# Kernel tuning notes

Hardware: AMD Instinct MI355X
Metric: run time of the kernel (lower is better)

## Reference

```python
import jax, jax.numpy as jnp
import numpy as np

HIDDEN = 2048
HEADS = 16
HEAD_DIM = HIDDEN // HEADS          # 128
HALF = HEAD_DIM // 2                # 64
LATENT = HIDDEN // 4                # 512 (compression_ratio=4)
ROPE_BASE = 10000.0


def _rope_cos_sin(seq_len):
    # LlamaRotaryEmbedding with dim=HALF
    inv_freq = 1.0 / (ROPE_BASE ** (jnp.arange(0, HALF, 2, dtype=jnp.float32) / HALF))
    t = jnp.arange(seq_len, dtype=jnp.float32)
    freqs = jnp.einsum('i,j->ij', t, inv_freq)          # [S, HALF/2]
    emb = jnp.concatenate([freqs, freqs], axis=-1)       # [S, HALF]
    cos = jnp.cos(emb)[None, :, None, :]                 # [1,S,1,HALF]
    sin = jnp.sin(emb)[None, :, None, :]
    return cos, sin


def _rotate_half(x):
    x1, x2 = jnp.split(x, 2, axis=-1)
    return jnp.concatenate([-x2, x1], axis=-1)


def _apply_rope(x, cos, sin):
    return x * cos + _rotate_half(x) * sin


def setup_inputs() -> dict:
    key = jax.random.key(0)
    ks = jax.random.split(key, 10)
    B, S = 2, 2048
    std = 0.02
    inp = {
        'x':        jax.random.normal(ks[0], (B, S, HIDDEN), jnp.float32),
        # weights stored as [in, out] (transposed torch Linear weight)
        'W_kv_d':   jax.random.normal(ks[1], (HIDDEN, LATENT), jnp.float32) * std,
        'W_q_d':    jax.random.normal(ks[2], (HIDDEN, LATENT), jnp.float32) * std,
        'W_k_u':    jax.random.normal(ks[3], (LATENT, HEADS * HALF), jnp.float32) * std,
        'W_q_u':    jax.random.normal(ks[4], (LATENT, HEADS * HALF), jnp.float32) * std,
        'W_v_u':    jax.random.normal(ks[5], (LATENT, HIDDEN), jnp.float32) * std,
        'W_rope_k': jax.random.normal(ks[6], (HIDDEN, HIDDEN // 2), jnp.float32) * std,
        'W_rope_q': jax.random.normal(ks[7], (LATENT, HIDDEN // 2), jnp.float32) * std,
        'W_o':      jax.random.normal(ks[8], (HIDDEN, HIDDEN), jnp.float32) * std,
    }
    return inp


def reference(x, W_kv_d, W_q_d, W_k_u, W_q_u, W_v_u, W_rope_k, W_rope_q, W_o):
    B, S, _ = x.shape
    kv_latent = x @ W_kv_d                      # [B,S,LATENT]
    q_latent = x @ W_q_d                        # [B,S,LATENT]

    k = (kv_latent @ W_k_u).reshape(B, S, HEADS, HALF)
    q = (q_latent @ W_q_u).reshape(B, S, HEADS, HALF)
    v = (kv_latent @ W_v_u).reshape(B, S, HEADS, HEAD_DIM)

    q_rope = (q_latent @ W_rope_q).reshape(B, S, HEADS, HALF)
    k_rope = (x @ W_rope_k).reshape(B, S, HEADS, HALF)

    cos, sin = _rope_cos_sin(S)
    k_rope = _apply_rope(k_rope, cos, sin)
    q_rope = _apply_rope(q_rope, cos, sin)

    q = jnp.concatenate([q, q_rope], axis=-1)   # [B,S,H,HEAD_DIM]
    k = jnp.concatenate([k, k_rope], axis=-1)

    scale = 1.0 / jnp.sqrt(jnp.float32(HEAD_DIM))
    scores = jnp.einsum('bqhd,bkhd->bhqk', q, k) * scale   # [B,H,S,S]
    causal = jnp.tril(jnp.ones((S, S), dtype=bool))
    scores = jnp.where(causal[None, None], scores, jnp.float32(-1e30))
    attn = jax.nn.softmax(scores, axis=-1)
    y = jnp.einsum('bhqk,bkhd->bqhd', attn, v).reshape(B, S, HIDDEN)
    return y @ W_o
```

## Files before the change

kernel.cpp:

```cpp
#include <hip/hip_runtime.h>
#include <hip/hip_bf16.h>

typedef __hip_bfloat16 bf16;
typedef __attribute__((ext_vector_type(8))) short short8;
typedef __attribute__((ext_vector_type(4))) float f32x4;

#define AS1 __attribute__((address_space(1)))
#define AS3 __attribute__((address_space(3)))

__device__ __forceinline__ void gload_lds16(const bf16* gp, bf16* lp) {
  __builtin_amdgcn_global_load_lds((const AS1 void*)gp, (AS3 void*)lp, 16, 0, 0);
}

__device__ __forceinline__ float fast_exp2(float x) {
#if __has_builtin(__builtin_amdgcn_exp2f)
  return __builtin_amdgcn_exp2f(x);
#else
  return exp2f(x);
#endif
}

__device__ __forceinline__ void store_c(bf16* C, size_t idx, float v) { C[idx] = __float2bfloat16(v); }
__device__ __forceinline__ void store_c(float* C, size_t idx, float v) { C[idx] = v; }

struct __align__(8) b16x4 { bf16 a, b, c, d; };

__global__ void cvt_f32_bf16(const float* __restrict__ in, bf16* __restrict__ out) {
  const int i = (blockIdx.x * 256 + threadIdx.x) * 4;
  const float4 v = *(const float4*)(in + i);
  out[i + 0] = __float2bfloat16(v.x);
  out[i + 1] = __float2bfloat16(v.y);
  out[i + 2] = __float2bfloat16(v.z);
  out[i + 3] = __float2bfloat16(v.w);
}

struct PrepArgs {
  const float* src[8];
  bf16* dst[8];
  int R[8], C[8], cum[8];
};

__global__ void prep_kernel(PrepArgs a) {
  __shared__ bf16 t[32][33];
  const int blk = blockIdx.x;
  int e = 0;
  while (e < 7 && blk >= a.cum[e]) ++e;
  const int lt = blk - (e ? a.cum[e - 1] : 0);
  const int R = a.R[e], C = a.C[e];
  const int tpr = C >> 5;
  const int bx = lt % tpr, by = lt / tpr;
  const float* in = a.src[e];
  bf16* out = a.dst[e];
  const int c0 = bx * 32, r0 = by * 32;
  const int tx = threadIdx.x, ty = threadIdx.y;
  for (int i = 0; i < 4; ++i)
    t[ty + 8 * i][tx] = __float2bfloat16(in[(size_t)(r0 + ty + 8 * i) * C + c0 + tx]);
  __syncthreads();
  for (int i = 0; i < 4; ++i)
    out[(size_t)(c0 + ty + 8 * i) * R + r0 + tx] = t[tx][ty + 8 * i];
}

template <typename CT, int MODE>
__global__ void gemm_bt(const bf16* __restrict__ A, int lda,
                        const bf16* __restrict__ Bt,
                        CT* __restrict__ C, bf16* __restrict__ C2, int ldc,
                        int K)
{
  __shared__ __align__(16) bf16 As[128 * 32];
  __shared__ __align__(16) bf16 Bs[128 * 32];
  const int tid  = threadIdx.x;
  const int wave = tid >> 6, lane = tid & 63;
  const int quad = lane >> 4, l16 = lane & 15;
  const int m0 = blockIdx.y * 128, n0 = blockIdx.x * 128;
  const int wm = (wave >> 1) * 64, wn = (wave & 1) * 64;

  f32x4 acc[4][4];
#pragma unroll
  for (int i = 0; i < 4; ++i)
#pragma unroll
    for (int j = 0; j < 4; ++j) acc[i][j] = (f32x4){0.f, 0.f, 0.f, 0.f};

  const int r1  = tid >> 2;
  const int ks1 = (tid & 3) * 8;

  for (int k0 = 0; k0 < K; k0 += 32) {
    gload_lds16(A  + (size_t)(m0 + r1)      * lda + k0 + ks1, &As[tid * 8]);
    gload_lds16(A  + (size_t)(m0 + r1 + 64) * lda + k0 + ks1, &As[(tid + 256) * 8]);
    gload_lds16(Bt + (size_t)(n0 + r1)      * K   + k0 + ks1, &Bs[tid * 8]);
    gload_lds16(Bt + (size_t)(n0 + r1 + 64) * K   + k0 + ks1, &Bs[(tid + 256) * 8]);
    __syncthreads();

    short8 af[4], bf_[4];
#pragma unroll
    for (int mt = 0; mt < 4; ++mt)
      af[mt] = *(const short8*)&As[(wm + mt * 16 + l16) * 32 + quad * 8];
#pragma unroll
    for (int nt = 0; nt < 4; ++nt)
      bf_[nt] = *(const short8*)&Bs[(wn + nt * 16 + l16) * 32 + quad * 8];
#pragma unroll
    for (int mt = 0; mt < 4; ++mt)
#pragma unroll
      for (int nt = 0; nt < 4; ++nt)
        acc[mt][nt] = __builtin_amdgcn_mfma_f32_16x16x32_bf16(af[mt], bf_[nt], acc[mt][nt], 0, 0, 0);
    __syncthreads();
  }

#pragma unroll
  for (int mt = 0; mt < 4; ++mt) {
    const int row = m0 + wm + mt * 16 + quad * 4;
#pragma unroll
    for (int nt = 0; nt < 4; ++nt) {
      const int cn = n0 + wn + nt * 16 + l16;
      const f32x4 v = acc[mt][nt];
      if (MODE == 0) {
#pragma unroll
        for (int r = 0; r < 4; ++r)
          store_c(C, (size_t)(row + r) * ldc + cn, v[r]);
      } else if (MODE == 4) {
        if (cn < 1024) {
#pragma unroll
          for (int r = 0; r < 4; ++r)
            store_c(C, (size_t)(row + r) * 1024 + cn, v[r]);
        } else {
          const int cn2 = cn - 1024;
          const int g = ((cn2 >> 6) << 7) + 64 + (cn2 & 63);
#pragma unroll
          for (int r = 0; r < 4; ++r)
            C2[(size_t)(row + r) * 2048 + g] = __float2bfloat16(v[r]);
        }
      }
    }
  }
}

__global__ void gemm_up_fused(const bf16* __restrict__ latcat,
                              const bf16* __restrict__ wtUP,
                              const bf16* __restrict__ wtQcat,
                              bf16* __restrict__ vT, bf16* __restrict__ kfull,
                              bf16* __restrict__ qfull)
{
  const bool is2 = (blockIdx.x >= 24);
  const bf16* A  = latcat + (is2 ? 512 : 0);
  const bf16* Bt = is2 ? wtQcat : wtUP;
  const int n0 = (is2 ? (int)blockIdx.x - 24 : (int)blockIdx.x) * 128;
  const int K = 512, lda = 1024;

  __shared__ __align__(16) bf16 As[128 * 32];
  __shared__ __align__(16) bf16 Bs[128 * 32];
  const int tid  = threadIdx.x;
  const int wave = tid >> 6, lane = tid & 63;
  const int quad = lane >> 4, l16 = lane & 15;
  const int m0 = blockIdx.y * 128;
  const int wm = (wave >> 1) * 64, wn = (wave & 1) * 64;

  f32x4 acc[4][4];
#pragma unroll
  for (int i = 0; i < 4; ++i)
#pragma unroll
    for (int j = 0; j < 4; ++j) acc[i][j] = (f32x4){0.f, 0.f, 0.f, 0.f};

  const int r1  = tid >> 2;
  const int ks1 = (tid & 3) * 8;

  for (int k0 = 0; k0 < K; k0 += 32) {
    gload_lds16(A  + (size_t)(m0 + r1)      * lda + k0 + ks1, &As[tid * 8]);
    gload_lds16(A  + (size_t)(m0 + r1 + 64) * lda + k0 + ks1, &As[(tid + 256) * 8]);
    gload_lds16(Bt + (size_t)(n0 + r1)      * K   + k0 + ks1, &Bs[tid * 8]);
    gload_lds16(Bt + (size_t)(n0 + r1 + 64) * K   + k0 + ks1, &Bs[(tid + 256) * 8]);
    __syncthreads();

    short8 af[4], bf_[4];
#pragma unroll
    for (int mt = 0; mt < 4; ++mt)
      af[mt] = *(const short8*)&As[(wm + mt * 16 + l16) * 32 + quad * 8];
#pragma unroll
    for (int nt = 0; nt < 4; ++nt)
      bf_[nt] = *(const short8*)&Bs[(wn + nt * 16 + l16) * 32 + quad * 8];
#pragma unroll
    for (int mt = 0; mt < 4; ++mt)
#pragma unroll
      for (int nt = 0; nt < 4; ++nt)
        acc[mt][nt] = __builtin_amdgcn_mfma_f32_16x16x32_bf16(af[mt], bf_[nt], acc[mt][nt], 0, 0, 0);
    __syncthreads();
  }

  if (is2) {
#pragma unroll
    for (int mt = 0; mt < 4; ++mt) {
      const int row = m0 + wm + mt * 16 + quad * 4;
#pragma unroll
      for (int nt = 0; nt < 4; ++nt) {
        const int cn = n0 + wn + nt * 16 + l16;
        const int g = (((cn >> 6) & 15) << 7) + ((cn >> 10) << 6) + (cn & 63);
        const f32x4 v = acc[mt][nt];
#pragma unroll
        for (int r = 0; r < 4; ++r)
          qfull[(size_t)(row + r) * 2048 + g] = __float2bfloat16(v[r]);
      }
    }
  } else {
#pragma unroll
    for (int mt = 0; mt < 4; ++mt) {
      const int row = m0 + wm + mt * 16 + quad * 4;
#pragma unroll
      for (int nt = 0; nt < 4; ++nt) {
        const int cn = n0 + wn + nt * 16 + l16;
        const f32x4 v = acc[mt][nt];
        if (cn < 1024) {
          const int g = ((cn >> 6) << 7) + (cn & 63);
#pragma unroll
          for (int r = 0; r < 4; ++r)
            kfull[(size_t)(row + r) * 2048 + g] = __float2bfloat16(v[r]);
        } else {
          const int cn2 = cn - 1024;
          const int bb = row >> 11, s0 = row & 2047;
          b16x4 pk;
          pk.a = __float2bfloat16(v[0]); pk.b = __float2bfloat16(v[1]);
          pk.c = __float2bfloat16(v[2]); pk.d = __float2bfloat16(v[3]);
          *(b16x4*)(vT + ((size_t)(bb * 2048 + cn2)) * 2048 + s0) = pk;
        }
      }
    }
  }
}

__global__ void rope_kernel(bf16* __restrict__ q, bf16* __restrict__ k)
{
  const int idx = blockIdx.x * 256 + threadIdx.x;
  const int i = idx & 31;
  const int h = (idx >> 5) & 15;
  const int s = (idx >> 9) & 2047;
  const int b = idx >> 20;
  const size_t off = ((size_t)(b * 2048 + s)) * 2048 + h * 128 + 64;
  const float inv = fast_exp2(-(float)i * 0.41524101186092029f);
  const float ang = (float)s * inv;
  const float cs = cosf(ang), sn = sinf(ang);
  {
    bf16* p = q + off;
    const float x1 = __bfloat162float(p[i]);
    const float x2 = __bfloat162float(p[i + 32]);
    p[i]      = __float2bfloat16(x1 * cs - x2 * sn);
    p[i + 32] = __float2bfloat16(x2 * cs + x1 * sn);
  }
  {
    bf16* p = k + off;
    const float x1 = __bfloat162float(p[i]);
    const float x2 = __bfloat162float(p[i + 32]);
    p[i]      = __float2bfloat16(x1 * cs - x2 * sn);
    p[i + 32] = __float2bfloat16(x2 * cs + x1 * sn);
  }
}

__global__ __launch_bounds__(256, 3) void attn6_kernel(
    const bf16* __restrict__ Q, const bf16* __restrict__ Kf,
    const bf16* __restrict__ VT, bf16* __restrict__ Y)
{
  __shared__ __align__(16) bf16 Ks[64][136];
  __shared__ __align__(16) bf16 VTs[128][72];
  __shared__ __align__(16) bf16 Ps[4][16][72];
  const int tid  = threadIdx.x;
  const int wave = tid >> 6, lane = tid & 63;
  const int quad = lane >> 4, l16 = lane & 15;
  const int bh = blockIdx.x;
  const int qt = 31 - blockIdx.y;
  const size_t kqbase = ((size_t)(bh >> 4) * 2048) * 2048 + (bh & 15) * 128;
  const size_t vtbase = (size_t)bh * 128 * 2048;
  const float C2 = 0.08838834764831845f * 1.4426950408889634f;
  const float MNEG = -30.0f;

  short8 ones;
#pragma unroll
  for (int i = 0; i < 8; ++i) ones[i] = (short)0x3F80;

  const int krow = tid >> 4, kcol = (tid & 15) * 8;
  const int vrow = tid >> 3, vcol = (tid & 7) * 8;

  const int q0 = qt * 64;
  const int T = qt + 1;
  const int row0q = q0 + wave * 16 + quad * 4;

  short8 qf[4];
  {
    const bf16* qp = Q + kqbase + (size_t)(q0 + wave * 16 + l16) * 2048 + quad * 8;
#pragma unroll
    for (int kc = 0; kc < 4; ++kc) qf[kc] = *(const short8*)(qp + kc * 32);
  }
  f32x4 o[8];
#pragma unroll
  for (int i = 0; i < 8; ++i) o[i] = (f32x4){0, 0, 0, 0};
  f32x4 lacc = (f32x4){0, 0, 0, 0};

  short8 kg[4], vg[4];
#pragma unroll
  for (int i = 0; i < 4; ++i)
    kg[i] = *(const short8*)(Kf + kqbase + (size_t)(krow + i * 16) * 2048 + kcol);
#pragma unroll
  for (int i = 0; i < 4; ++i)
    vg[i] = *(const short8*)(VT + vtbase + (size_t)(vrow + i * 32) * 2048 + vcol);

  for (int t = 0; t < T; ++t) {
    const int k0 = t * 64;
    __syncthreads();
#pragma unroll
    for (int i = 0; i < 4; ++i) *(short8*)&Ks[krow + i * 16][kcol] = kg[i];
#pragma unroll
    for (int i = 0; i < 4; ++i) *(short8*)&VTs[vrow + i * 32][vcol] = vg[i];
    __syncthreads();
    if (t + 1 < T) {
      const int kn = k0 + 64;
#pragma unroll
      for (int i = 0; i < 4; ++i)
        kg[i] = *(const short8*)(Kf + kqbase + (size_t)(kn + krow + i * 16) * 2048 + kcol);
#pragma unroll
      for (int i = 0; i < 4; ++i)
        vg[i] = *(const short8*)(VT + vtbase + (size_t)(vrow + i * 32) * 2048 + kn + vcol);
    }

    f32x4 sf[4];
#pragma unroll
    for (int kt = 0; kt < 4; ++kt) {
      f32x4 a = (f32x4){0, 0, 0, 0};
#pragma unroll
      for (int kc = 0; kc < 4; ++kc) {
        const short8 bfr = *(const short8*)&Ks[kt * 16 + l16][kc * 32 + quad * 8];
        a = __builtin_amdgcn_mfma_f32_16x16x32_bf16(qf[kc], bfr, a, 0, 0, 0);
      }
      sf[kt] = a;
    }
    if (t == T - 1) {
#pragma unroll
      for (int kt = 0; kt < 4; ++kt) {
        const int col = k0 + kt * 16 + l16;
#pragma unroll
        for (int r = 0; r < 4; ++r)
          sf[kt][r] = (col > row0q + r) ? -3e38f : sf[kt][r];
      }
    }
#pragma unroll
    for (int kt = 0; kt < 4; ++kt)
#pragma unroll
      for (int r = 0; r < 4; ++r) {
        const float p = fast_exp2(__builtin_fmaf(sf[kt][r], C2, MNEG));
        Ps[wave][quad * 4 + r][kt * 16 + l16] = __float2bfloat16(p);
      }
    asm volatile("s_waitcnt lgkmcnt(0)" ::: "memory");
#pragma unroll
    for (int kc = 0; kc < 2; ++kc) {
      const short8 ap = *(const short8*)&Ps[wave][l16][kc * 32 + quad * 8];
      lacc = __builtin_amdgcn_mfma_f32_16x16x32_bf16(ap, ones, lacc, 0, 0, 0);
#pragma unroll
      for (int dt = 0; dt < 8; ++dt) {
        const short8 vb = *(const short8*)&VTs[dt * 16 + l16][kc * 32 + quad * 8];
        o[dt] = __builtin_amdgcn_mfma_f32_16x16x32_bf16(ap, vb, o[dt], 0, 0, 0);
      }
    }
  }

#pragma unroll
  for (int r = 0; r < 4; ++r) {
    const float inv = 1.0f / lacc[r];
#pragma unroll
    for (int dt = 0; dt < 8; ++dt)
      Y[kqbase + (size_t)(row0q + r) * 2048 + dt * 16 + l16] = __float2bfloat16(o[dt][r] * inv);
  }
}

extern "C" void kernel_launch(void* const* d_in, const int* in_sizes, int n_in,
                              void* d_out, int out_size, void* d_ws, size_t ws_size,
                              hipStream_t stream)
{
  const float* x      = (const float*)d_in[0];
  const float* Wkvd   = (const float*)d_in[1];
  const float* Wqd    = (const float*)d_in[2];
  const float* Wku    = (const float*)d_in[3];
  const float* Wqu    = (const float*)d_in[4];
  const float* Wvu    = (const float*)d_in[5];
  const float* Wropek = (const float*)d_in[6];
  const float* Wropeq = (const float*)d_in[7];
  const float* Wo     = (const float*)d_in[8];

  char* ws = (char*)d_ws;
  size_t off = 0;
  auto alloc = [&](size_t elems) {
    bf16* p = (bf16*)(ws + off);
    off += ((elems * sizeof(bf16) + 255) & ~(size_t)255);
    return p;
  };
  bf16* wtX    = alloc((size_t)2048 * 2048);
  bf16* wtUP   = alloc((size_t)3072 * 512);
  bf16* wtQcat = alloc((size_t)2048 * 512);
  bf16* latcat = alloc((size_t)4096 * 1024);
  bf16* wt_o   = alloc((size_t)2048 * 2048);
  bf16* xbf    = alloc((size_t)4096 * 2048);
  bf16* qfull  = alloc((size_t)4096 * 2048);
  bf16* kfull  = alloc((size_t)4096 * 2048);
  bf16* ybuf   = (bf16*)ws;
  bf16* vT     = (bf16*)d_out;
  (void)ws_size; (void)in_sizes; (void)n_in; (void)out_size;

  cvt_f32_bf16<<<8192, 256, 0, stream>>>(x, xbf);

  PrepArgs pa;
  const float* srcs[8] = {Wkvd, Wqd, Wropek, Wku, Wvu, Wqu, Wropeq, Wo};
  bf16* dsts[8] = {wtX, wtX + (size_t)512 * 2048, wtX + (size_t)1024 * 2048,
                   wtUP, wtUP + (size_t)1024 * 512,
                   wtQcat, wtQcat + (size_t)1024 * 512, wt_o};
  const int Rs[8] = {2048, 2048, 2048, 512, 512, 512, 512, 2048};
  const int Cs[8] = {512, 512, 1024, 1024, 2048, 1024, 1024, 2048};
  int cum = 0;
  for (int e = 0; e < 8; ++e) {
    pa.src[e] = srcs[e]; pa.dst[e] = dsts[e]; pa.R[e] = Rs[e]; pa.C[e] = Cs[e];
    cum += (Rs[e] >> 5) * (Cs[e] >> 5);
    pa.cum[e] = cum;
  }
  prep_kernel<<<cum, dim3(32, 8), 0, stream>>>(pa);

  gemm_bt<bf16, 4><<<dim3(16, 32), 256, 0, stream>>>(xbf, 2048, wtX, latcat, kfull, 1024, 2048);
  gemm_up_fused<<<dim3(40, 32), 256, 0, stream>>>(latcat, wtUP, wtQcat, vT, kfull, qfull);

  rope_kernel<<<(2 * 2048 * 16 * 32) / 256, 256, 0, stream>>>(qfull, kfull);
  attn6_kernel<<<dim3(32, 32), 256, 0, stream>>>(qfull, kfull, vT, ybuf);
  gemm_bt<float, 0><<<dim3(16, 32), 256, 0, stream>>>(ybuf, 2048, wt_o, (float*)d_out, (bf16*)nullptr, 2048, 2048);
}
```

Baseline: 328.9 us.

## Use 32-row-per-wave attention tiles and 64x128 GEMM tiles

The attention kernel moves to 2 waves per block, and each wave now handles two 16-row query sets. Every K and V fragment read from LDS therefore feeds two MFMAs, which halves LDS traffic per unit of math. The cost is more accumulator registers per thread and fewer waves per block, and launch bounds are relaxed to allow that. The projection and output GEMMs switch from 128x128 to 64x128 tiles, doubling the grid for better CU load balance at the cost of less data reuse per tile.

```diff
diff --git a/kernel.cpp b/kernel.cpp
--- a/kernel.cpp
+++ b/kernel.cpp
@@ -61,22 +61,22 @@
 }
 
 template <typename CT, int MODE>
-__global__ void gemm_bt(const bf16* __restrict__ A, int lda,
-                        const bf16* __restrict__ Bt,
-                        CT* __restrict__ C, bf16* __restrict__ C2, int ldc,
-                        int K)
+__global__ void gemm_bt64(const bf16* __restrict__ A, int lda,
+                          const bf16* __restrict__ Bt,
+                          CT* __restrict__ C, bf16* __restrict__ C2, int ldc,
+                          int K)
 {
-  __shared__ __align__(16) bf16 As[128 * 32];
+  __shared__ __align__(16) bf16 As[64 * 32];
   __shared__ __align__(16) bf16 Bs[128 * 32];
   const int tid  = threadIdx.x;
   const int wave = tid >> 6, lane = tid & 63;
   const int quad = lane >> 4, l16 = lane & 15;
-  const int m0 = blockIdx.y * 128, n0 = blockIdx.x * 128;
-  const int wm = (wave >> 1) * 64, wn = (wave & 1) * 64;
-
-  f32x4 acc[4][4];
-#pragma unroll
-  for (int i = 0; i < 4; ++i)
+  const int m0 = blockIdx.y * 64, n0 = blockIdx.x * 128;
+  const int wm = (wave >> 1) * 32, wn = (wave & 1) * 64;
+
+  f32x4 acc[2][4];
+#pragma unroll
+  for (int i = 0; i < 2; ++i)
 #pragma unroll
     for (int j = 0; j < 4; ++j) acc[i][j] = (f32x4){0.f, 0.f, 0.f, 0.f};
 
@@ -85,20 +85,19 @@
 
   for (int k0 = 0; k0 < K; k0 += 32) {
     gload_lds16(A  + (size_t)(m0 + r1)      * lda + k0 + ks1, &As[tid * 8]);
-    gload_lds16(A  + (size_t)(m0 + r1 + 64) * lda + k0 + ks1, &As[(tid + 256) * 8]);
     gload_lds16(Bt + (size_t)(n0 + r1)      * K   + k0 + ks1, &Bs[tid * 8]);
     gload_lds16(Bt + (size_t)(n0 + r1 + 64) * K   + k0 + ks1, &Bs[(tid + 256) * 8]);
     __syncthreads();
 
-    short8 af[4], bf_[4];
-#pragma unroll
-    for (int mt = 0; mt < 4; ++mt)
+    short8 af[2], bf_[4];
+#pragma unroll
+    for (int mt = 0; mt < 2; ++mt)
       af[mt] = *(const short8*)&As[(wm + mt * 16 + l16) * 32 + quad * 8];
 #pragma unroll
     for (int nt = 0; nt < 4; ++nt)
       bf_[nt] = *(const short8*)&Bs[(wn + nt * 16 + l16) * 32 + quad * 8];
 #pragma unroll
-    for (int mt = 0; mt < 4; ++mt)
+    for (int mt = 0; mt < 2; ++mt)
 #pragma unroll
       for (int nt = 0; nt < 4; ++nt)
         acc[mt][nt] = __builtin_amdgcn_mfma_f32_16x16x32_bf16(af[mt], bf_[nt], acc[mt][nt], 0, 0, 0);
@@ -106,7 +105,7 @@
   }
 
 #pragma unroll
-  for (int mt = 0; mt < 4; ++mt) {
+  for (int mt = 0; mt < 2; ++mt) {
     const int row = m0 + wm + mt * 16 + quad * 4;
 #pragma unroll
     for (int nt = 0; nt < 4; ++nt) {
@@ -116,7 +115,7 @@
 #pragma unroll
         for (int r = 0; r < 4; ++r)
           store_c(C, (size_t)(row + r) * ldc + cn, v[r]);
-      } else if (MODE == 4) {
+      } else {
         if (cn < 1024) {
 #pragma unroll
           for (int r = 0; r < 4; ++r)
@@ -251,13 +250,13 @@
   }
 }
 
-__global__ __launch_bounds__(256, 3) void attn6_kernel(
+__global__ __launch_bounds__(128, 1) void attn7_kernel(
     const bf16* __restrict__ Q, const bf16* __restrict__ Kf,
     const bf16* __restrict__ VT, bf16* __restrict__ Y)
 {
   __shared__ __align__(16) bf16 Ks[64][136];
   __shared__ __align__(16) bf16 VTs[128][72];
-  __shared__ __align__(16) bf16 Ps[4][16][72];
+  __shared__ __align__(16) bf16 Ps[2][32][72];
   const int tid  = threadIdx.x;
   const int wave = tid >> 6, lane = tid & 63;
   const int quad = lane >> 4, l16 = lane & 15;
@@ -277,91 +276,110 @@
 
   const int q0 = qt * 64;
   const int T = qt + 1;
-  const int row0q = q0 + wave * 16 + quad * 4;
-
-  short8 qf[4];
-  {
-    const bf16* qp = Q + kqbase + (size_t)(q0 + wave * 16 + l16) * 2048 + quad * 8;
-#pragma unroll
-    for (int kc = 0; kc < 4; ++kc) qf[kc] = *(const short8*)(qp + kc * 32);
-  }
-  f32x4 o[8];
-#pragma unroll
-  for (int i = 0; i < 8; ++i) o[i] = (f32x4){0, 0, 0, 0};
-  f32x4 lacc = (f32x4){0, 0, 0, 0};
-
-  short8 kg[4], vg[4];
-#pragma unroll
-  for (int i = 0; i < 4; ++i)
-    kg[i] = *(const short8*)(Kf + kqbase + (size_t)(krow + i * 16) * 2048 + kcol);
-#pragma unroll
-  for (int i = 0; i < 4; ++i)
-    vg[i] = *(const short8*)(VT + vtbase + (size_t)(vrow + i * 32) * 2048 + vcol);
+
+  short8 qf[2][4];
+#pragma unroll
+  for (int set = 0; set < 2; ++set) {
+    const bf16* qp = Q + kqbase + (size_t)(q0 + wave * 32 + set * 16 + l16) * 2048 + quad * 8;
+#pragma unroll
+    for (int kc = 0; kc < 4; ++kc) qf[set][kc] = *(const short8*)(qp + kc * 32);
+  }
+  f32x4 o[2][8];
+#pragma unroll
+  for (int s = 0; s < 2; ++s)
+#pragma unroll
+    for (int i = 0; i < 8; ++i) o[s][i] = (f32x4){0, 0, 0, 0};
+  f32x4 lacc[2];
+  lacc[0] = (f32x4){0, 0, 0, 0};
+  lacc[1] = (f32x4){0, 0, 0, 0};
+
+  short8 kg[8], vg[8];
+#pragma unroll
+  for (int i = 0; i < 8; ++i)
+    kg[i] = *(const short8*)(Kf + kqbase + (size_t)(krow + i * 8) * 2048 + kcol);
+#pragma unroll
+  for (int i = 0; i < 8; ++i)
+    vg[i] = *(const short8*)(VT + vtbase + (size_t)(vrow + i * 16) * 2048 + vcol);
 
   for (int t = 0; t < T; ++t) {
     const int k0 = t * 64;
     __syncthreads();
 #pragma unroll
-    for (int i = 0; i < 4; ++i) *(short8*)&Ks[krow + i * 16][kcol] = kg[i];
-#pragma unroll
-    for (int i = 0; i < 4; ++i) *(short8*)&VTs[vrow + i * 32][vcol] = vg[i];
+    for (int i = 0; i < 8; ++i) *(short8*)&Ks[krow + i * 8][kcol] = kg[i];
+#pragma unroll
+    for (int i = 0; i < 8; ++i) *(short8*)&VTs[vrow + i * 16][vcol] = vg[i];
     __syncthreads();
     if (t + 1 < T) {
       const int kn = k0 + 64;
 #pragma unroll
-      for (int i = 0; i < 4; ++i)
-        kg[i] = *(const short8*)(Kf + kqbase + (size_t)(kn + krow + i * 16) * 2048 + kcol);
-#pragma unroll
-      for (int i = 0; i < 4; ++i)
-        vg[i] = *(const short8*)(VT + vtbase + (size_t)(vrow + i * 32) * 2048 + kn + vcol);
-    }
-
-    f32x4 sf[4];
-#pragma unroll
-    for (int kt = 0; kt < 4; ++kt) {
-      f32x4 a = (f32x4){0, 0, 0, 0};
-#pragma unroll
-      for (int kc = 0; kc < 4; ++kc) {
+      for (int i = 0; i < 8; ++i)
+        kg[i] = *(const short8*)(Kf + kqbase + (size_t)(kn + krow + i * 8) * 2048 + kcol);
+#pragma unroll
+      for (int i = 0; i < 8; ++i)
+        vg[i] = *(const short8*)(VT + vtbase + (size_t)(vrow + i * 16) * 2048 + kn + vcol);
+    }
+
+    f32x4 sf[2][4];
+#pragma unroll
+    for (int s = 0; s < 2; ++s)
+#pragma unroll
+      for (int kt = 0; kt < 4; ++kt) sf[s][kt] = (f32x4){0, 0, 0, 0};
+#pragma unroll
+    for (int kc = 0; kc < 4; ++kc)
+#pragma unroll
+      for (int kt = 0; kt < 4; ++kt) {
         const short8 bfr = *(const short8*)&Ks[kt * 16 + l16][kc * 32 + quad * 8];
-        a = __builtin_amdgcn_mfma_f32_16x16x32_bf16(qf[kc], bfr, a, 0, 0, 0);
-      }
-      sf[kt] = a;
-    }
+        sf[0][kt] = __builtin_amdgcn_mfma_f32_16x16x32_bf16(qf[0][kc], bfr, sf[0][kt], 0, 0, 0);
+        sf[1][kt] = __builtin_amdgcn_mfma_f32_16x16x32_bf16(qf[1][kc], bfr, sf[1][kt], 0, 0, 0);
+      }
     if (t == T - 1) {
 #pragma unroll
-      for (int kt = 0; kt < 4; ++kt) {
-        const int col = k0 + kt * 16 + l16;
-#pragma unroll
-        for (int r = 0; r < 4; ++r)
-          sf[kt][r] = (col > row0q + r) ? -3e38f : sf[kt][r];
-      }
-    }
-#pragma unroll
-    for (int kt = 0; kt < 4; ++kt)
-#pragma unroll
-      for (int r = 0; r < 4; ++r) {
-        const float p = fast_exp2(__builtin_fmaf(sf[kt][r], C2, MNEG));
-        Ps[wave][quad * 4 + r][kt * 16 + l16] = __float2bfloat16(p);
-      }
+      for (int s = 0; s < 2; ++s) {
+        const int row0 = q0 + wave * 32 + s * 16 + quad * 4;
+#pragma unroll
+        for (int kt = 0; kt < 4; ++kt) {
+          const int col = k0 + kt * 16 + l16;
+#pragma unroll
+          for (int r = 0; r < 4; ++r)
+            sf[s][kt][r] = (col > row0 + r) ? -3e38f : sf[s][kt][r];
+        }
+      }
+    }
+#pragma unroll
+    for (int s = 0; s < 2; ++s)
+#pragma unroll
+      for (int kt = 0; kt < 4; ++kt)
+#pragma unroll
+        for (int r = 0; r < 4; ++r) {
+          const float p = fast_exp2(__builtin_fmaf(sf[s][kt][r], C2, MNEG));
+          Ps[wave][s * 16 + quad * 4 + r][kt * 16 + l16] = __float2bfloat16(p);
+        }
     asm volatile("s_waitcnt lgkmcnt(0)" ::: "memory");
 #pragma unroll
     for (int kc = 0; kc < 2; ++kc) {
-      const short8 ap = *(const short8*)&Ps[wave][l16][kc * 32 + quad * 8];
-      lacc = __builtin_amdgcn_mfma_f32_16x16x32_bf16(ap, ones, lacc, 0, 0, 0);
+      const short8 ap0 = *(const short8*)&Ps[wave][l16][kc * 32 + quad * 8];
+      const short8 ap1 = *(const short8*)&Ps[wave][16 + l16][kc * 32 + quad * 8];
+      lacc[0] = __builtin_amdgcn_mfma_f32_16x16x32_bf16(ap0, ones, lacc[0], 0, 0, 0);
+      lacc[1] = __builtin_amdgcn_mfma_f32_16x16x32_bf16(ap1, ones, lacc[1], 0, 0, 0);
 #pragma unroll
       for (int dt = 0; dt < 8; ++dt) {
         const short8 vb = *(const short8*)&VTs[dt * 16 + l16][kc * 32 + quad * 8];
-        o[dt] = __builtin_amdgcn_mfma_f32_16x16x32_bf16(ap, vb, o[dt], 0, 0, 0);
-      }
-    }
-  }
-
-#pragma unroll
-  for (int r = 0; r < 4; ++r) {
-    const float inv = 1.0f / lacc[r];
-#pragma unroll
-    for (int dt = 0; dt < 8; ++dt)
-      Y[kqbase + (size_t)(row0q + r) * 2048 + dt * 16 + l16] = __float2bfloat16(o[dt][r] * inv);
+        o[0][dt] = __builtin_amdgcn_mfma_f32_16x16x32_bf16(ap0, vb, o[0][dt], 0, 0, 0);
+        o[1][dt] = __builtin_amdgcn_mfma_f32_16x16x32_bf16(ap1, vb, o[1][dt], 0, 0, 0);
+      }
+    }
+  }
+
+#pragma unroll
+  for (int s = 0; s < 2; ++s) {
+    const int row0 = q0 + wave * 32 + s * 16 + quad * 4;
+#pragma unroll
+    for (int r = 0; r < 4; ++r) {
+      const float inv = 1.0f / lacc[s][r];
+#pragma unroll
+      for (int dt = 0; dt < 8; ++dt)
+        Y[kqbase + (size_t)(row0 + r) * 2048 + dt * 16 + l16] = __float2bfloat16(o[s][dt][r] * inv);
+    }
   }
 }
 
@@ -415,10 +433,10 @@
   }
   prep_kernel<<<cum, dim3(32, 8), 0, stream>>>(pa);
 
-  gemm_bt<bf16, 4><<<dim3(16, 32), 256, 0, stream>>>(xbf, 2048, wtX, latcat, kfull, 1024, 2048);
+  gemm_bt64<bf16, 4><<<dim3(16, 64), 256, 0, stream>>>(xbf, 2048, wtX, latcat, kfull, 1024, 2048);
   gemm_up_fused<<<dim3(40, 32), 256, 0, stream>>>(latcat, wtUP, wtQcat, vT, kfull, qfull);
 
   rope_kernel<<<(2 * 2048 * 16 * 32) / 256, 256, 0, stream>>>(qfull, kfull);
-  attn6_kernel<<<dim3(32, 32), 256, 0, stream>>>(qfull, kfull, vT, ybuf);
-  gemm_bt<float, 0><<<dim3(16, 32), 256, 0, stream>>>(ybuf, 2048, wt_o, (float*)d_out, (bf16*)nullptr, 2048, 2048);
-}
+  attn7_kernel<<<dim3(32, 32), 128, 0, stream>>>(qfull, kfull, vT, ybuf);
+  gemm_bt64<float, 0><<<dim3(16, 64), 256, 0, stream>>>(ybuf, 2048, wt_o, (float*)d_out, (bf16*)nullptr, 2048, 2048);
+}
```

Measured after the change: 350.7 us. +6.6%, slower.
